# Kernel optimization log

Measured on AMD Instinct MI355X. Metric: run time of the kernel, lower is better.

Reference implementation:

```python
import jax, jax.numpy as jnp
import numpy as np

B, OBJ, INP, HID = 8, 128, 64, 256
D = 3 * INP  # concatenated per-object feature dim


def setup_inputs() -> dict:
    key = jax.random.key(0)
    ks = jax.random.split(key, 12)
    s = 0.02
    return {
        "x0": jax.random.normal(ks[0], (B, OBJ, INP), jnp.float32),
        "x1": jax.random.normal(ks[1], (B, OBJ, INP), jnp.float32),
        "x2": jax.random.normal(ks[2], (B, OBJ, INP), jnp.float32),
        # weights stored [in, out] so forward is x @ w + b
        "w_enc": jax.random.normal(ks[3], (2 * D, HID), jnp.float32) * s,
        "b_enc": jnp.zeros((HID,), jnp.float32),
        "w1": jax.random.normal(ks[4], (HID, HID), jnp.float32) * s,
        "b1": jnp.zeros((HID,), jnp.float32),
        "w2": jax.random.normal(ks[5], (HID, HID), jnp.float32) * s,
        "b2": jnp.zeros((HID,), jnp.float32),
        "w3": jax.random.normal(ks[6], (HID, HID), jnp.float32) * s,
        "b3": jnp.zeros((HID,), jnp.float32),
        "wd1": jax.random.normal(ks[7], (HID, HID), jnp.float32) * s,
        "bd1": jnp.zeros((HID,), jnp.float32),
        "wd2": jax.random.normal(ks[8], (HID, INP), jnp.float32) * s,
        "bd2": jnp.zeros((INP,), jnp.float32),
    }


def reference(x0, x1, x2, w_enc, b_enc, w1, b1, w2, b2, w3, b3, wd1, bd1, wd2, bd2):
    x = jnp.concatenate([x0, x1, x2], axis=-1)  # [B, N, D]
    # Fused equivalent of Linear(cat(e1, e2)): split w_enc rows into the part
    # acting on the first-object features and the second-object features, then
    # broadcast-add instead of materializing the [B,N,N,2D] concat tensor.
    ea = jnp.einsum("bnd,dh->bnh", x, w_enc[:D])   # acts on data_e1
    eb = jnp.einsum("bnd,dh->bnh", x, w_enc[D:])   # acts on data_e2
    h = jax.nn.relu(ea[:, :, None, :] + eb[:, None, :, :] + b_enc)  # [B,N,N,H]
    h = jax.nn.relu(h @ w1 + b1)
    h = jax.nn.relu(h @ w2 + b2)
    h = h @ w3 + b3              # fc3 has no activation before the mean
    pooled = h.mean(axis=2)      # [B, N, H]
    out = jax.nn.relu(pooled @ wd1 + bd1) @ wd2 + bd2  # [B, N, INP]
    return out
```

## Files before the change

kernel.cpp:

```cpp
#include <hip/hip_runtime.h>
#include <stdint.h>


#define HID 256
#define NOBJ 128
#define NROW 1024

typedef __attribute__((ext_vector_type(8))) short short8;
typedef __attribute__((ext_vector_type(4))) float float4v;
typedef __attribute__((ext_vector_type(16))) float float16v;
typedef __attribute__((ext_vector_type(2))) unsigned int uint2v;

__device__ __forceinline__ unsigned int f2bf_u(float f) {
    unsigned int u = __builtin_bit_cast(unsigned int, f);
    u += 0x7fffu + ((u >> 16) & 1u);
    return u >> 16;
}
__device__ __forceinline__ unsigned int pack2(float a, float b) {
    return f2bf_u(a) | (f2bf_u(b) << 16);
}
__device__ __forceinline__ float relu(float v) { return v > 0.f ? v : 0.f; }

__device__ __forceinline__ void lds_barrier() {
    asm volatile("s_waitcnt lgkmcnt(0)\n\ts_barrier" ::: "memory");
}

__global__ void setup_kernel(const float* __restrict__ x0, const float* __restrict__ x1,
                             const float* __restrict__ x2, const float* __restrict__ w_enc,
                             const float* __restrict__ b_enc,
                             const float* __restrict__ w1, const float* __restrict__ w2,
                             const float* __restrict__ w3, const float* __restrict__ b3,
                             const float* __restrict__ wd1, const float* __restrict__ bd1,
                             unsigned short* __restrict__ wt,
                             float* __restrict__ ea, float* __restrict__ eb,
                             float* __restrict__ W34, float* __restrict__ b34) {
    const int bx = blockIdx.x, t = threadIdx.x;
    __shared__ float lw[256][33];
    __shared__ float xs[2][192];
    if (bx < 16) {
        const int m = bx >> 3, tau = bx & 7;
        const float* w = (m == 0) ? w1 : w2;
        const int n = t & 31, kk = t >> 5;
#pragma unroll
        for (int rep = 0; rep < 32; ++rep) {
            int k = rep * 8 + kk;
            lw[k][n] = w[k * 256 + tau * 32 + n];
        }
        __syncthreads();
        unsigned short* outp = wt + (m * 8 + tau) * 8192;
        const int lane = t & 63, wq = t >> 6;
        const int h5 = lane >> 5, l31n = lane & 31;
#pragma unroll
        for (int rep = 0; rep < 4; ++rep) {
            const int kb = wq * 4 + rep;
            short8 v;
#pragma unroll
            for (int e = 0; e < 8; ++e)
                v[e] = (short)f2bf_u(lw[kb * 16 + h5 * 8 + e][l31n]);
            *(short8*)(outp + kb * 512 + lane * 8) = v;
        }
        return;
    }
    if (bx < 528) {
        const int e = bx - 16;
        for (int idx = t; idx < 384; idx += 256) {
            int r = idx / 192, d = idx % 192;
            int row = e * 2 + r;
            float v = (d < 64) ? x0[row * 64 + d]
                    : (d < 128) ? x1[row * 64 + d - 64]
                    : x2[row * 64 + d - 128];
            xs[r][d] = v;
        }
        __syncthreads();
        float aA[2] = {0.f, 0.f}, aB[2] = {0.f, 0.f};
#pragma unroll 16
        for (int d = 0; d < 192; ++d) {
            float wa = w_enc[d * 256 + t];
            float wb = w_enc[(192 + d) * 256 + t];
#pragma unroll
            for (int r = 0; r < 2; ++r) { aA[r] += xs[r][d] * wa; aB[r] += xs[r][d] * wb; }
        }
        float be = b_enc[t];
#pragma unroll
        for (int r = 0; r < 2; ++r) {
            ea[(e * 2 + r) * 256 + t] = aA[r] + be;
            eb[(e * 2 + r) * 256 + t] = aB[r];
        }
        return;
    }
    if (bx < 784) {
        const int m = bx - 528;
        float a = 0.f;
#pragma unroll 8
        for (int k = 0; k < 256; ++k) a += w3[m * 256 + k] * wd1[k * 256 + t];
        W34[m * 256 + t] = a;
        return;
    }
    {
        float a = bd1[t];
#pragma unroll 8
        for (int k = 0; k < 256; ++k) a += b3[k] * wd1[k * 256 + t];
        b34[t] = a;
    }
}

__global__ __launch_bounds__(256, 2) void pair_kernel(
        const float* __restrict__ ea, const float* __restrict__ eb,
        const unsigned short* __restrict__ wt,
        const float* __restrict__ b1, const float* __restrict__ b2,
        float* __restrict__ msg) {
    __shared__ __align__(16) unsigned short hbuf[128 * 256];
    __shared__ float ms[HID];

    const int w = blockIdx.x, b = w >> 7;
    const int t = threadIdx.x, wv = t >> 6, lane = t & 63;
    const int l31 = lane & 31, h5 = lane >> 5;
    const int n0 = wv * 64;

    const unsigned short* aptr = wt + lane * 8;

    short8 af[4][2], bfr[2][4];
#pragma unroll
    for (int pg = 0; pg < 3; ++pg) {
        af[pg][0] = *(const short8*)(aptr + ((wv * 2 + 0) * 16 + pg) * 512);
        af[pg][1] = *(const short8*)(aptr + ((wv * 2 + 1) * 16 + pg) * 512);
    }

    {
        const float4v va = *(const float4v*)(ea + w * 256 + lane * 4);
        const float* ebbase = eb + (b * NOBJ) * 256;
        const int c = lane >> 1, sub = (lane & 1) * 4;
#pragma unroll 4
        for (int jj = 0; jj < 32; ++jj) {
            const int j = wv * 32 + jj;
            float4v vb = *(const float4v*)(ebbase + j * 256 + lane * 4);
            int addr = j * 256 + ((c ^ (j & 31)) << 3) + sub;
            *(uint2v*)(hbuf + addr) = (uint2v){
                pack2(relu(va[0] + vb[0]), relu(va[1] + vb[1])),
                pack2(relu(va[2] + vb[2]), relu(va[3] + vb[3]))};
        }
    }
    lds_barrier();

    int jb[4];
#pragma unroll
    for (int tj = 0; tj < 4; ++tj) jb[tj] = (tj * 32 + l31) * 256;
#pragma unroll
    for (int tj = 0; tj < 4; ++tj)
        bfr[0][tj] = *(const short8*)(hbuf + jb[tj] + ((h5 ^ l31) << 3));

    float16v acc[2][4];

#pragma unroll
    for (int l = 0; l < 2; ++l) {
        const float* bias = (l == 0) ? b1 : b2;
#pragma unroll
        for (int tn = 0; tn < 2; ++tn)
#pragma unroll
            for (int q = 0; q < 4; ++q) {
                float4v bv = *(const float4v*)(bias + n0 + tn * 32 + q * 8 + h5 * 4);
#pragma unroll
                for (int i = 0; i < 4; ++i)
#pragma unroll
                    for (int tj = 0; tj < 4; ++tj)
                        acc[tn][tj][q * 4 + i] = bv[i];
            }
#pragma unroll
        for (int kb = 0; kb < 16; ++kb) {
            const int g = l * 16 + kb, gp = g + 3;
            if (gp < 32) {
                const int lp = gp >> 4, kp = gp & 15;
                af[gp & 3][0] = *(const short8*)(aptr + ((lp * 8 + wv * 2 + 0) * 16 + kp) * 512);
                af[gp & 3][1] = *(const short8*)(aptr + ((lp * 8 + wv * 2 + 1) * 16 + kp) * 512);
            }
            if (kb < 15) {
                const int off = ((((kb + 1) * 2 + h5) ^ l31) << 3);
#pragma unroll
                for (int tj = 0; tj < 4; ++tj)
                    bfr[(kb + 1) & 1][tj] = *(const short8*)(hbuf + jb[tj] + off);
            }
#pragma unroll
            for (int tn = 0; tn < 2; ++tn)
#pragma unroll
                for (int tj = 0; tj < 4; ++tj)
                    acc[tn][tj] = __builtin_amdgcn_mfma_f32_32x32x16_bf16(
                        af[g & 3][tn], bfr[kb & 1][tj], acc[tn][tj], 0, 0, 0);
        }

        if (l == 0) {
            lds_barrier();
#pragma unroll
            for (int tn = 0; tn < 2; ++tn)
#pragma unroll
                for (int q = 0; q < 4; ++q) {
                    const int nb_ = n0 + tn * 32 + 8 * q + 4 * h5;
                    const int cn = nb_ >> 3, sub = nb_ & 7;
#pragma unroll
                    for (int tj = 0; tj < 4; ++tj) {
                        const int j = tj * 32 + l31;
                        int addr = j * 256 + ((cn ^ l31) << 3) + sub;
                        *(uint2v*)(hbuf + addr) = (uint2v){
                            pack2(relu(acc[tn][tj][q * 4]), relu(acc[tn][tj][q * 4 + 1])),
                            pack2(relu(acc[tn][tj][q * 4 + 2]), relu(acc[tn][tj][q * 4 + 3]))};
                    }
                }
            lds_barrier();
#pragma unroll
            for (int tj = 0; tj < 4; ++tj)
                bfr[0][tj] = *(const short8*)(hbuf + jb[tj] + ((h5 ^ l31) << 3));
        }
    }

#pragma unroll
    for (int tn = 0; tn < 2; ++tn)
#pragma unroll
        for (int r = 0; r < 16; ++r) {
            float s = relu(acc[tn][0][r]) + relu(acc[tn][1][r])
                    + relu(acc[tn][2][r]) + relu(acc[tn][3][r]);
            s += __shfl_xor(s, 1);
            s += __shfl_xor(s, 2);
            s += __shfl_xor(s, 4);
            s += __shfl_xor(s, 8);
            s += __shfl_xor(s, 16);
            if (l31 == 0) {
                const int n = n0 + tn * 32 + (r & 3) + 8 * (r >> 2) + 4 * h5;
                ms[n] = s * 0.0078125f;
            }
        }
    __syncthreads();
    if (t < 64)
        *(float4v*)(msg + w * 256 + t * 4) = *(const float4v*)(ms + t * 4);
}

__global__ __launch_bounds__(512) void decoder_kernel(
        const float* __restrict__ msg, const float* __restrict__ W34,
        const float* __restrict__ b34, const float* __restrict__ wd2,
        const float* __restrict__ bd2, float* __restrict__ out) {
    __shared__ float ml[4][256];
    __shared__ float ps[2][4][256];
    __shared__ float tl[4][256];
    __shared__ float p2[2][4][64];
    const int bx = blockIdx.x, t = threadIdx.x;
    const int r0 = bx * 4;

#pragma unroll
    for (int i = t; i < 1024; i += 512) ml[i >> 8][i & 255] = msg[r0 * 256 + i];
    __syncthreads();

    {
        const int n = t & 255, kh = t >> 8;
        float a0 = 0.f, a1 = 0.f, a2 = 0.f, a3 = 0.f;
        const float* wp = W34 + (kh * 128) * 256 + n;
        const float* m0 = &ml[0][kh * 128];
        const float* m1 = &ml[1][kh * 128];
        const float* m2r = &ml[2][kh * 128];
        const float* m3 = &ml[3][kh * 128];
#pragma unroll 16
        for (int k = 0; k < 128; ++k) {
            const float wv_ = wp[k * 256];
            a0 += m0[k] * wv_;
            a1 += m1[k] * wv_;
            a2 += m2r[k] * wv_;
            a3 += m3[k] * wv_;
        }
        ps[kh][0][n] = a0; ps[kh][1][n] = a1; ps[kh][2][n] = a2; ps[kh][3][n] = a3;
    }
    __syncthreads();
#pragma unroll
    for (int i = t; i < 1024; i += 512) {
        const int r = i >> 8, nn = i & 255;
        tl[r][nn] = relu(ps[0][r][nn] + ps[1][r][nn] + b34[nn]);
    }
    __syncthreads();

    {
        const int o = t & 63, rr = (t >> 6) & 3, kh = t >> 8;
        float a = 0.f;
        const float* w2p = wd2 + (kh * 128) * 64 + o;
        const float* tp = &tl[rr][kh * 128];
#pragma unroll 16
        for (int k = 0; k < 128; ++k) a += tp[k] * w2p[k * 64];
        p2[kh][rr][o] = a;
    }
    __syncthreads();
    if (t < 256) {
        const int o = t & 63, r = t >> 6;
        out[(r0 + r) * 64 + o] = p2[0][r][o] + p2[1][r][o] + bd2[o];
    }
}

extern "C" void kernel_launch(void* const* d_in, const int* in_sizes, int n_in,
                              void* d_out, int out_size, void* d_ws, size_t ws_size,
                              hipStream_t stream) {
    const float* x0    = (const float*)d_in[0];
    const float* x1    = (const float*)d_in[1];
    const float* x2    = (const float*)d_in[2];
    const float* w_enc = (const float*)d_in[3];
    const float* b_enc = (const float*)d_in[4];
    const float* w1    = (const float*)d_in[5];
    const float* b1    = (const float*)d_in[6];
    const float* w2    = (const float*)d_in[7];
    const float* b2    = (const float*)d_in[8];
    const float* w3    = (const float*)d_in[9];
    const float* b3    = (const float*)d_in[10];
    const float* wd1   = (const float*)d_in[11];
    const float* bd1   = (const float*)d_in[12];
    const float* wd2   = (const float*)d_in[13];
    const float* bd2   = (const float*)d_in[14];
    float* out = (float*)d_out;

    unsigned short* wt = (unsigned short*)d_ws;
    float* ea  = (float*)((char*)d_ws + 3 * 65536 * sizeof(unsigned short));
    float* eb  = ea + NROW * HID;
    float* W34 = eb + NROW * HID;
    float* b34 = W34 + 256 * 256;
    float* msg = b34 + 256;

    setup_kernel<<<785, 256, 0, stream>>>(x0, x1, x2, w_enc, b_enc, w1, w2,
                                          w3, b3, wd1, bd1, wt, ea, eb, W34, b34);
    pair_kernel<<<NROW, 256, 0, stream>>>(ea, eb, wt, b1, b2, msg);
    decoder_kernel<<<NROW / 4, 512, 0, stream>>>(msg, W34, b34, wd2, bd2, out);
}
```

Measured before the change: 154.5 us.

## Split pair kernel across eight waves with 32-column tiles per wave

Doubles the pair kernel block to 512 threads so each wave computes a 32-wide output slice instead of 64, halving accumulator and A-fragment registers per wave. Intended to raise the number of resident waves and hide MFMA/LDS latency. In exchange, every LDS-loaded B fragment is reused by fewer MFMAs, total LDS read traffic doubles, and the B-fragment double-buffer prefetch is removed.

```diff
diff --git a/kernel.cpp b/kernel.cpp
--- a/kernel.cpp
+++ b/kernel.cpp
@@ -104,7 +104,7 @@
     }
 }
 
-__global__ __launch_bounds__(256, 2) void pair_kernel(
+__global__ __launch_bounds__(512, 4) void pair_kernel(
         const float* __restrict__ ea, const float* __restrict__ eb,
         const unsigned short* __restrict__ wt,
         const float* __restrict__ b1, const float* __restrict__ b2,
@@ -115,24 +115,22 @@
     const int w = blockIdx.x, b = w >> 7;
     const int t = threadIdx.x, wv = t >> 6, lane = t & 63;
     const int l31 = lane & 31, h5 = lane >> 5;
-    const int n0 = wv * 64;
+    const int n0 = wv * 32;
 
     const unsigned short* aptr = wt + lane * 8;
 
-    short8 af[4][2], bfr[2][4];
-#pragma unroll
-    for (int pg = 0; pg < 3; ++pg) {
-        af[pg][0] = *(const short8*)(aptr + ((wv * 2 + 0) * 16 + pg) * 512);
-        af[pg][1] = *(const short8*)(aptr + ((wv * 2 + 1) * 16 + pg) * 512);
-    }
+    short8 af[4], bfr[4];
+#pragma unroll
+    for (int pg = 0; pg < 3; ++pg)
+        af[pg] = *(const short8*)(aptr + (wv * 16 + pg) * 512);
 
     {
         const float4v va = *(const float4v*)(ea + w * 256 + lane * 4);
         const float* ebbase = eb + (b * NOBJ) * 256;
         const int c = lane >> 1, sub = (lane & 1) * 4;
 #pragma unroll 4
-        for (int jj = 0; jj < 32; ++jj) {
-            const int j = wv * 32 + jj;
+        for (int jj = 0; jj < 16; ++jj) {
+            const int j = wv * 16 + jj;
             float4v vb = *(const float4v*)(ebbase + j * 256 + lane * 4);
             int addr = j * 256 + ((c ^ (j & 31)) << 3) + sub;
             *(uint2v*)(hbuf + addr) = (uint2v){
@@ -145,88 +143,73 @@
     int jb[4];
 #pragma unroll
     for (int tj = 0; tj < 4; ++tj) jb[tj] = (tj * 32 + l31) * 256;
-#pragma unroll
-    for (int tj = 0; tj < 4; ++tj)
-        bfr[0][tj] = *(const short8*)(hbuf + jb[tj] + ((h5 ^ l31) << 3));
-
-    float16v acc[2][4];
+
+    float16v acc[4];
 
 #pragma unroll
     for (int l = 0; l < 2; ++l) {
         const float* bias = (l == 0) ? b1 : b2;
 #pragma unroll
-        for (int tn = 0; tn < 2; ++tn)
-#pragma unroll
-            for (int q = 0; q < 4; ++q) {
-                float4v bv = *(const float4v*)(bias + n0 + tn * 32 + q * 8 + h5 * 4);
-#pragma unroll
-                for (int i = 0; i < 4; ++i)
-#pragma unroll
-                    for (int tj = 0; tj < 4; ++tj)
-                        acc[tn][tj][q * 4 + i] = bv[i];
-            }
+        for (int q = 0; q < 4; ++q) {
+            float4v bv = *(const float4v*)(bias + n0 + q * 8 + h5 * 4);
+#pragma unroll
+            for (int i = 0; i < 4; ++i)
+#pragma unroll
+                for (int tj = 0; tj < 4; ++tj)
+                    acc[tj][q * 4 + i] = bv[i];
+        }
 #pragma unroll
         for (int kb = 0; kb < 16; ++kb) {
             const int g = l * 16 + kb, gp = g + 3;
             if (gp < 32) {
                 const int lp = gp >> 4, kp = gp & 15;
-                af[gp & 3][0] = *(const short8*)(aptr + ((lp * 8 + wv * 2 + 0) * 16 + kp) * 512);
-                af[gp & 3][1] = *(const short8*)(aptr + ((lp * 8 + wv * 2 + 1) * 16 + kp) * 512);
+                af[gp & 3] = *(const short8*)(aptr + ((lp * 8 + wv) * 16 + kp) * 512);
             }
-            if (kb < 15) {
-                const int off = ((((kb + 1) * 2 + h5) ^ l31) << 3);
+            {
+                const int off = (((kb * 2 + h5) ^ l31) << 3);
 #pragma unroll
                 for (int tj = 0; tj < 4; ++tj)
-                    bfr[(kb + 1) & 1][tj] = *(const short8*)(hbuf + jb[tj] + off);
+                    bfr[tj] = *(const short8*)(hbuf + jb[tj] + off);
             }
 #pragma unroll
-            for (int tn = 0; tn < 2; ++tn)
-#pragma unroll
-                for (int tj = 0; tj < 4; ++tj)
-                    acc[tn][tj] = __builtin_amdgcn_mfma_f32_32x32x16_bf16(
-                        af[g & 3][tn], bfr[kb & 1][tj], acc[tn][tj], 0, 0, 0);
+            for (int tj = 0; tj < 4; ++tj)
+                acc[tj] = __builtin_amdgcn_mfma_f32_32x32x16_bf16(
+                    af[g & 3], bfr[tj], acc[tj], 0, 0, 0);
         }
 
         if (l == 0) {
             lds_barrier();
 #pragma unroll
-            for (int tn = 0; tn < 2; ++tn)
-#pragma unroll
-                for (int q = 0; q < 4; ++q) {
-                    const int nb_ = n0 + tn * 32 + 8 * q + 4 * h5;
-                    const int cn = nb_ >> 3, sub = nb_ & 7;
-#pragma unroll
-                    for (int tj = 0; tj < 4; ++tj) {
-                        const int j = tj * 32 + l31;
-                        int addr = j * 256 + ((cn ^ l31) << 3) + sub;
-                        *(uint2v*)(hbuf + addr) = (uint2v){
-                            pack2(relu(acc[tn][tj][q * 4]), relu(acc[tn][tj][q * 4 + 1])),
-                            pack2(relu(acc[tn][tj][q * 4 + 2]), relu(acc[tn][tj][q * 4 + 3]))};
-                    }
+            for (int q = 0; q < 4; ++q) {
+                const int nb_ = n0 + 8 * q + 4 * h5;
+                const int cn = nb_ >> 3, sub = nb_ & 7;
+#pragma unroll
+                for (int tj = 0; tj < 4; ++tj) {
+                    const int j = tj * 32 + l31;
+                    int addr = j * 256 + ((cn ^ l31) << 3) + sub;
+                    *(uint2v*)(hbuf + addr) = (uint2v){
+                        pack2(relu(acc[tj][q * 4]), relu(acc[tj][q * 4 + 1])),
+                        pack2(relu(acc[tj][q * 4 + 2]), relu(acc[tj][q * 4 + 3]))};
                 }
+            }
             lds_barrier();
-#pragma unroll
-            for (int tj = 0; tj < 4; ++tj)
-                bfr[0][tj] = *(const short8*)(hbuf + jb[tj] + ((h5 ^ l31) << 3));
-        }
-    }
-
-#pragma unroll
-    for (int tn = 0; tn < 2; ++tn)
-#pragma unroll
-        for (int r = 0; r < 16; ++r) {
-            float s = relu(acc[tn][0][r]) + relu(acc[tn][1][r])
-                    + relu(acc[tn][2][r]) + relu(acc[tn][3][r]);
-            s += __shfl_xor(s, 1);
-            s += __shfl_xor(s, 2);
-            s += __shfl_xor(s, 4);
-            s += __shfl_xor(s, 8);
-            s += __shfl_xor(s, 16);
-            if (l31 == 0) {
-                const int n = n0 + tn * 32 + (r & 3) + 8 * (r >> 2) + 4 * h5;
-                ms[n] = s * 0.0078125f;
-            }
-        }
+        }
+    }
+
+#pragma unroll
+    for (int r = 0; r < 16; ++r) {
+        float s = relu(acc[0][r]) + relu(acc[1][r])
+                + relu(acc[2][r]) + relu(acc[3][r]);
+        s += __shfl_xor(s, 1);
+        s += __shfl_xor(s, 2);
+        s += __shfl_xor(s, 4);
+        s += __shfl_xor(s, 8);
+        s += __shfl_xor(s, 16);
+        if (l31 == 0) {
+            const int n = n0 + (r & 3) + 8 * (r >> 2) + 4 * h5;
+            ms[n] = s * 0.0078125f;
+        }
+    }
     __syncthreads();
     if (t < 64)
         *(float4v*)(msg + w * 256 + t * 4) = *(const float4v*)(ms + t * 4);
@@ -318,6 +301,6 @@
 
     setup_kernel<<<785, 256, 0, stream>>>(x0, x1, x2, w_enc, b_enc, w1, w2,
                                           w3, b3, wd1, bd1, wt, ea, eb, W34, b34);
-    pair_kernel<<<NROW, 256, 0, stream>>>(ea, eb, wt, b1, b2, msg);
+    pair_kernel<<<NROW, 512, 0, stream>>>(ea, eb, wt, b1, b2, msg);
     decoder_kernel<<<NROW / 4, 512, 0, stream>>>(msg, W34, b34, wd2, bd2, out);
 }
```

Result: faster. 147.2 us (-4.7%).
